# Performance work log

Hardware: AMD Instinct MI355X
Metric: run time of the kernel (lower is better)

## Reference

```python
import jax, jax.numpy as jnp
import numpy as np

B, N, C = 32, 1000, 81
MAX_INST = 100
MIN_CONF = 0.7
NMS_THRESH = 0.3
WINDOW = (0.0, 0.0, 1.0, 1.0)  # normalized y1, x1, y2, x2


def _apply_deltas(boxes, deltas):
    # boxes, deltas: [N, 4] in (y1, x1, y2, x2) / (dy, dx, log_dh, log_dw)
    h = boxes[:, 2] - boxes[:, 0]
    w = boxes[:, 3] - boxes[:, 1]
    cy = boxes[:, 0] + 0.5 * h + deltas[:, 0] * h
    cx = boxes[:, 1] + 0.5 * w + deltas[:, 1] * w
    h = h * jnp.exp(deltas[:, 2])
    w = w * jnp.exp(deltas[:, 3])
    y1 = cy - 0.5 * h
    x1 = cx - 0.5 * w
    return jnp.stack([y1, x1, y1 + h, x1 + w], axis=1)


def _clip_boxes(boxes, window):
    wy1, wx1, wy2, wx2 = window
    return jnp.stack([
        jnp.clip(boxes[:, 0], wy1, wy2),
        jnp.clip(boxes[:, 1], wx1, wx2),
        jnp.clip(boxes[:, 2], wy1, wy2),
        jnp.clip(boxes[:, 3], wx1, wx2)], axis=1)


def _pairwise_iou(b):
    y1, x1, y2, x2 = b[:, 0], b[:, 1], b[:, 2], b[:, 3]
    area = (y2 - y1) * (x2 - x1)
    iy = jnp.maximum(jnp.minimum(y2[:, None], y2[None, :]) - jnp.maximum(y1[:, None], y1[None, :]), 0.0)
    ix = jnp.maximum(jnp.minimum(x2[:, None], x2[None, :]) - jnp.maximum(x1[:, None], x1[None, :]), 0.0)
    inter = iy * ix
    union = area[:, None] + area[None, :] - inter
    return inter / jnp.maximum(union, 1e-8)


def _refine_one(rois, probs, deltas, std_dev):
    n = rois.shape[0]
    class_ids = jnp.argmax(probs, axis=1)                 # [N]
    scores = jnp.max(probs, axis=1)                       # [N]
    # per-roi deltas for the predicted class, scaled by bbox_std_dev
    d = jnp.take_along_axis(deltas, class_ids[:, None, None], axis=1)[:, 0, :] * std_dev
    boxes = _clip_boxes(_apply_deltas(rois, d), WINDOW)   # [N, 4]
    valid = (class_ids > 0) & (scores >= MIN_CONF)        # drop background + low conf

    # sort by score descending (invalid at the end)
    order = jnp.argsort(-jnp.where(valid, scores, -jnp.inf))
    b = boxes[order]
    s = scores[order]
    c = class_ids[order]
    v = valid[order]

    # greedy per-class NMS on score-sorted boxes
    iou = _pairwise_iou(b)                                # [N, N]
    sup = (iou > NMS_THRESH) & (c[:, None] == c[None, :])
    idx = jnp.arange(n)

    def step(keep, i):
        row = sup[i] & (idx > i) & keep[i]
        return keep & ~row, None

    keep, _ = jax.lax.scan(step, v, jnp.arange(n))
    keep = jax.lax.stop_gradient(keep)

    # kept boxes are already score-ordered -> compact first MAX_INST into slots
    slot = jnp.where(keep, jnp.cumsum(keep) - 1, MAX_INST)
    slot = jnp.minimum(slot, MAX_INST)                    # overflow bucket
    rows = jnp.concatenate([b, c[:, None].astype(b.dtype), s[:, None]], axis=1)  # [N, 6]
    out = jnp.zeros((MAX_INST + 1, 6), b.dtype).at[slot].set(rows)[:MAX_INST]
    return out                                            # [MAX_INST, 6]


def setup_inputs() -> dict:
    key = jax.random.key(0)
    k1, k2, k3, k4, k5 = jax.random.split(key, 5)
    cy = jax.random.uniform(k1, (B, N))
    cx = jax.random.uniform(k2, (B, N))
    h = jax.random.uniform(k3, (B, N), minval=0.02, maxval=0.4)
    w = jax.random.uniform(k4, (B, N), minval=0.02, maxval=0.4)
    rois = jnp.stack([
        jnp.clip(cy - 0.5 * h, 0.0, 1.0),
        jnp.clip(cx - 0.5 * w, 0.0, 1.0),
        jnp.clip(cy + 0.5 * h, 0.0, 1.0),
        jnp.clip(cx + 0.5 * w, 0.0, 1.0)], axis=2).astype(jnp.float32)
    logits = jax.random.normal(k5, (B, N, C), dtype=jnp.float32) * 2.0
    mrcnn_class = jax.nn.softmax(logits, axis=-1)
    mrcnn_bbox = jax.random.normal(jax.random.fold_in(key, 7), (B, N, C, 4), dtype=jnp.float32)
    bbox_std_dev = jnp.array([0.1, 0.1, 0.2, 0.2], dtype=jnp.float32)
    return {"rois": rois, "mrcnn_class": mrcnn_class, "mrcnn_bbox": mrcnn_bbox, "bbox_std_dev": bbox_std_dev}


def reference(rois, mrcnn_class, mrcnn_bbox, bbox_std_dev):
    out = jax.vmap(lambda r, p, d: _refine_one(r, p, d, bbox_std_dev))(rois, mrcnn_class, mrcnn_bbox)
    return out.reshape(B, MAX_INST, 6)
```

## Files before the change

### kernel.cpp

```cpp
#include <hip/hip_runtime.h>
#include <math.h>

#define BB 32
#define NN 1000
#define CC 81
#define MAX_INST 100
#define MIN_CONF 0.7f
#define NMS_THRESH 0.3f
#define MCAP 1024
#define RCHUNK 192
#define WMAX 16


__global__ __launch_bounds__(256) void roi_kernel(
    const float* __restrict__ rois,
    const float* __restrict__ probs,
    const float* __restrict__ deltas,
    const float* __restrict__ std_dev,
    float* __restrict__ glist,
    float* __restrict__ out)
{
  if (blockIdx.x == 0) {
    float4* o4 = (float4*)out;
    for (int i = threadIdx.x; i < BB * MAX_INST * 6 / 4; i += 256)
      o4[i] = make_float4(0.f, 0.f, 0.f, 0.f);
  }

  int wg = blockIdx.x * 4 + (threadIdx.x >> 6);
  if (wg >= BB * NN) return;
  int lane = threadIdx.x & 63;

  const float* p = probs + (size_t)wg * CC;
  float v = p[lane];
  int   c = lane;
  if (lane + 64 < CC) {
    float v2 = p[lane + 64];
    if (v2 > v) { v = v2; c = lane + 64; }
  }
  for (int off = 32; off; off >>= 1) {
    float vo = __shfl_down(v, off);
    int   co = __shfl_down(c, off);
    if (vo > v || (vo == v && co < c)) { v = vo; c = co; }
  }

  if (lane == 0) {
    float4* o = (float4*)(glist + (size_t)wg * 8);
    bool valid = (c > 0) && (v >= MIN_CONF);
    if (valid) {
      float4 dd = *(const float4*)(deltas + ((size_t)wg * CC + c) * 4);
      float4 r4 = *(const float4*)(rois + (size_t)wg * 4);
      float dy = dd.x * std_dev[0], dx = dd.y * std_dev[1];
      float dh = dd.z * std_dev[2], dw = dd.w * std_dev[3];
      float h = r4.z - r4.x, w = r4.w - r4.y;
      float cy = r4.x + 0.5f * h + dy * h;
      float cx = r4.y + 0.5f * w + dx * w;
      h *= expf(dh); w *= expf(dw);
      float y1 = cy - 0.5f * h, x1 = cx - 0.5f * w;
      float y2 = y1 + h,        x2 = x1 + w;
      y1 = fminf(fmaxf(y1, 0.f), 1.f); x1 = fminf(fmaxf(x1, 0.f), 1.f);
      y2 = fminf(fmaxf(y2, 0.f), 1.f); x2 = fminf(fmaxf(x2, 0.f), 1.f);
      o[0] = make_float4(y1, x1, y2, x2);
    }
    int b = wg / NN, n = wg - b * NN;
    o[1] = make_float4(valid ? v : -1.0f, (float)c, (float)n, 0.f);
  }
}

__global__ __launch_bounds__(256) void nms_kernel(
    const float* __restrict__ glist,
    float* __restrict__ out)
{
  const int b = blockIdx.x, t = threadIdx.x;

  __shared__ int   lcnt;
  __shared__ float cscore[MCAP];
  __shared__ int   cidx[MCAP];
  __shared__ float sy1[MCAP], sx1[MCAP], sy2[MCAP], sx2[MCAP];
  __shared__ int   scls[MCAP];
  __shared__ float sscr[MCAP];
  __shared__ unsigned long long rows[RCHUNK][WMAX];
  __shared__ unsigned long long keepw[WMAX];

  const float* base = glist + (size_t)b * NN * 8;

  if (t == 0) lcnt = 0;
  __syncthreads();

  for (int e = t; e < NN; e += 256) {
    const float4 s = ((const float4*)(base + (size_t)e * 8))[1];
    if (s.x >= 0.f) {
      int pos = atomicAdd(&lcnt, 1);
      cscore[pos] = s.x;
      cidx[pos]   = e;
    }
  }
  __syncthreads();

  const int M = lcnt;
  const int W = (M + 63) >> 6;

  for (int e = t; e < M; e += 256) {
    float sc = cscore[e]; int oi = cidx[e];
    int r = 0;
    for (int j = 0; j < M; ++j) {
      float sj = cscore[j]; int ij = cidx[j];
      if (sj > sc || (sj == sc && ij < oi)) ++r;
    }
    const float4 a = ((const float4*)(base + (size_t)oi * 8))[0];
    const float4 s = ((const float4*)(base + (size_t)oi * 8))[1];
    sy1[r] = a.x; sx1[r] = a.y; sy2[r] = a.z; sx2[r] = a.w;
    scls[r] = (int)s.y; sscr[r] = sc;
  }
  if (t < WMAX) {
    unsigned long long kw = 0ULL;
    int nb = M - t * 64;
    if (nb > 0) kw = (nb >= 64) ? ~0ULL : ((1ULL << nb) - 1ULL);
    keepw[t] = kw;
  }
  __syncthreads();

  const int wv = t >> 6, lane = t & 63;
  for (int c0 = 0; c0 < M; c0 += RCHUNK) {
    int R = min(RCHUNK, M - c0);
    for (int task = wv; task < R * W; task += 4) {
      int i = c0 + task / W;
      int w = task % W;
      int j = w * 64 + lane;
      bool cond = false;
      float iy1 = sy1[i], ix1 = sx1[i], iy2 = sy2[i], ix2 = sx2[i];
      int ic = scls[i];
      if (j < M && j > i && scls[j] == ic) {
        float jy1 = sy1[j], jx1 = sx1[j], jy2 = sy2[j], jx2 = sx2[j];
        float ai = (iy2 - iy1) * (ix2 - ix1);
        float aj = (jy2 - jy1) * (jx2 - jx1);
        float iy = fmaxf(fminf(iy2, jy2) - fmaxf(iy1, jy1), 0.f);
        float ix = fmaxf(fminf(ix2, jx2) - fmaxf(ix1, jx1), 0.f);
        float inter = iy * ix;
        float uni = fmaxf(ai + aj - inter, 1e-8f);
        cond = (inter / uni) > NMS_THRESH;
      }
      unsigned long long word = __ballot(cond);
      if (lane == 0) rows[task / W][w] = word;
    }
    __syncthreads();
    if (t < 64) {
      unsigned long long kw = (t < W) ? keepw[t] : 0ULL;
      for (int i = c0; i < c0 + R; ++i) {
        unsigned long long kwi = __shfl((long long)kw, i >> 6);
        if ((kwi >> (i & 63)) & 1ULL) {
          if (t < W) kw &= ~rows[i - c0][t];
        }
      }
      if (t < W) keepw[t] = kw;
    }
    __syncthreads();
  }

  for (int r = t; r < M; r += 256) {
    unsigned long long kwme = keepw[r >> 6];
    if ((kwme >> (r & 63)) & 1ULL) {
      int slot = 0;
      for (int w = 0; w < (r >> 6); ++w) slot += __popcll(keepw[w]);
      slot += __popcll(kwme & ((1ULL << (r & 63)) - 1ULL));
      if (slot < MAX_INST) {
        float* o = out + ((size_t)b * MAX_INST + slot) * 6;
        o[0] = sy1[r]; o[1] = sx1[r]; o[2] = sy2[r]; o[3] = sx2[r];
        o[4] = (float)scls[r]; o[5] = sscr[r];
      }
    }
  }
}

extern "C" void kernel_launch(void* const* d_in, const int* in_sizes, int n_in,
                              void* d_out, int out_size, void* d_ws, size_t ws_size,
                              hipStream_t stream) {
  const float* rois    = (const float*)d_in[0];
  const float* probs   = (const float*)d_in[1];
  const float* deltas  = (const float*)d_in[2];
  const float* std_dev = (const float*)d_in[3];
  float* out = (float*)d_out;

  float* glist = (float*)d_ws;

  roi_kernel<<<(BB * NN + 3) / 4, 256, 0, stream>>>(rois, probs, deltas, std_dev,
                                                    glist, out);
  nms_kernel<<<BB, 256, 0, stream>>>(glist, out);
}
```

Measured before the change: 103.8 us.

## Split ROI output into SoA buffers, use half-wave argmax, add single-wave NMS path

The ROI kernel now reduces each row over 32 lanes instead of 64, so 8 rows are processed per block. It writes scores, classes and boxes into separate struct-of-arrays buffers rather than an interleaved 8-float record. The NMS kernel loads scores as float4 vectors, zeroes its own slice of the output, and uses a serial single-wave greedy path with no block barriers when at most 64 candidates survive. Together these aim to cut memory traffic, launch work and synchronisation. The fast path only runs when the candidate count is small, which depends on the input distribution.

```diff
diff --git a/kernel.cpp b/kernel.cpp
--- a/kernel.cpp
+++ b/kernel.cpp
@@ -17,35 +17,32 @@
     const float* __restrict__ probs,
     const float* __restrict__ deltas,
     const float* __restrict__ std_dev,
-    float* __restrict__ glist,
-    float* __restrict__ out)
+    float* __restrict__ sval,
+    int* __restrict__ gcls,
+    float4* __restrict__ gbox)
 {
-  if (blockIdx.x == 0) {
-    float4* o4 = (float4*)out;
-    for (int i = threadIdx.x; i < BB * MAX_INST * 6 / 4; i += 256)
-      o4[i] = make_float4(0.f, 0.f, 0.f, 0.f);
-  }
-
-  int wg = blockIdx.x * 4 + (threadIdx.x >> 6);
+  int wg = blockIdx.x * 8 + (threadIdx.x >> 5);
   if (wg >= BB * NN) return;
-  int lane = threadIdx.x & 63;
+  int hl = threadIdx.x & 31;
 
   const float* p = probs + (size_t)wg * CC;
-  float v = p[lane];
-  int   c = lane;
-  if (lane + 64 < CC) {
-    float v2 = p[lane + 64];
-    if (v2 > v) { v = v2; c = lane + 64; }
-  }
-  for (int off = 32; off; off >>= 1) {
+  float v = p[hl];
+  int   c = hl;
+  float v2 = p[hl + 32];
+  if (v2 > v) { v = v2; c = hl + 32; }
+  if (hl < CC - 64) {
+    float v3 = p[hl + 64];
+    if (v3 > v) { v = v3; c = hl + 64; }
+  }
+  for (int off = 16; off; off >>= 1) {
     float vo = __shfl_down(v, off);
     int   co = __shfl_down(c, off);
     if (vo > v || (vo == v && co < c)) { v = vo; c = co; }
   }
 
-  if (lane == 0) {
-    float4* o = (float4*)(glist + (size_t)wg * 8);
+  if (hl == 0) {
     bool valid = (c > 0) && (v >= MIN_CONF);
+    sval[wg] = valid ? v : -1.0f;
     if (valid) {
       float4 dd = *(const float4*)(deltas + ((size_t)wg * CC + c) * 4);
       float4 r4 = *(const float4*)(rois + (size_t)wg * 4);
@@ -59,58 +56,102 @@
       float y2 = y1 + h,        x2 = x1 + w;
       y1 = fminf(fmaxf(y1, 0.f), 1.f); x1 = fminf(fmaxf(x1, 0.f), 1.f);
       y2 = fminf(fmaxf(y2, 0.f), 1.f); x2 = fminf(fmaxf(x2, 0.f), 1.f);
-      o[0] = make_float4(y1, x1, y2, x2);
-    }
-    int b = wg / NN, n = wg - b * NN;
-    o[1] = make_float4(valid ? v : -1.0f, (float)c, (float)n, 0.f);
+      gcls[wg] = c;
+      gbox[wg] = make_float4(y1, x1, y2, x2);
+    }
   }
 }
 
 __global__ __launch_bounds__(256) void nms_kernel(
-    const float* __restrict__ glist,
+    const float* __restrict__ sval,
+    const int* __restrict__ gcls,
+    const float4* __restrict__ gbox,
     float* __restrict__ out)
 {
   const int b = blockIdx.x, t = threadIdx.x;
 
   __shared__ int   lcnt;
-  __shared__ float cscore[MCAP];
-  __shared__ int   cidx[MCAP];
+  __shared__ float lscore[MCAP];
+  __shared__ int   lidx[MCAP];
   __shared__ float sy1[MCAP], sx1[MCAP], sy2[MCAP], sx2[MCAP];
-  __shared__ int   scls[MCAP];
+  __shared__ int   scl[MCAP];
   __shared__ float sscr[MCAP];
   __shared__ unsigned long long rows[RCHUNK][WMAX];
   __shared__ unsigned long long keepw[WMAX];
 
-  const float* base = glist + (size_t)b * NN * 8;
+  float4* ob4 = (float4*)(out + (size_t)b * MAX_INST * 6);
+  for (int i = t; i < MAX_INST * 6 / 4; i += 256)
+    ob4[i] = make_float4(0.f, 0.f, 0.f, 0.f);
 
   if (t == 0) lcnt = 0;
   __syncthreads();
 
-  for (int e = t; e < NN; e += 256) {
-    const float4 s = ((const float4*)(base + (size_t)e * 8))[1];
-    if (s.x >= 0.f) {
-      int pos = atomicAdd(&lcnt, 1);
-      cscore[pos] = s.x;
-      cidx[pos]   = e;
-    }
+  const float4* sv4 = (const float4*)(sval + (size_t)b * NN);
+  if (t < NN / 4) {
+    float4 s4 = sv4[t];
+    if (s4.x >= 0.f) { int q = atomicAdd(&lcnt, 1); lscore[q] = s4.x; lidx[q] = 4 * t + 0; }
+    if (s4.y >= 0.f) { int q = atomicAdd(&lcnt, 1); lscore[q] = s4.y; lidx[q] = 4 * t + 1; }
+    if (s4.z >= 0.f) { int q = atomicAdd(&lcnt, 1); lscore[q] = s4.z; lidx[q] = 4 * t + 2; }
+    if (s4.w >= 0.f) { int q = atomicAdd(&lcnt, 1); lscore[q] = s4.w; lidx[q] = 4 * t + 3; }
   }
   __syncthreads();
 
   const int M = lcnt;
-  const int W = (M + 63) >> 6;
+  const size_t boff = (size_t)b * NN;
 
   for (int e = t; e < M; e += 256) {
-    float sc = cscore[e]; int oi = cidx[e];
+    float sc = lscore[e]; int oi = lidx[e];
     int r = 0;
     for (int j = 0; j < M; ++j) {
-      float sj = cscore[j]; int ij = cidx[j];
+      float sj = lscore[j]; int ij = lidx[j];
       if (sj > sc || (sj == sc && ij < oi)) ++r;
     }
-    const float4 a = ((const float4*)(base + (size_t)oi * 8))[0];
-    const float4 s = ((const float4*)(base + (size_t)oi * 8))[1];
+    float4 a = gbox[boff + oi];
     sy1[r] = a.x; sx1[r] = a.y; sy2[r] = a.z; sx2[r] = a.w;
-    scls[r] = (int)s.y; sscr[r] = sc;
-  }
+    scl[r] = gcls[boff + oi]; sscr[r] = sc;
+  }
+  __syncthreads();
+
+  if (M <= 64) {
+    if (t < 64) {
+      const int j = t;
+      float jy1 = 0.f, jx1 = 0.f, jy2 = 0.f, jx2 = 0.f, aj = 0.f, jscr = 0.f;
+      int jc = -1;
+      if (j < M) {
+        jy1 = sy1[j]; jx1 = sx1[j]; jy2 = sy2[j]; jx2 = sx2[j];
+        jc = scl[j]; jscr = sscr[j];
+        aj = (jy2 - jy1) * (jx2 - jx1);
+      }
+      unsigned long long keep = (M >= 64) ? ~0ULL : ((1ULL << M) - 1ULL);
+      for (int i = 0; i < M; ++i) {
+        if ((keep >> i) & 1ULL) {
+          float iy1 = sy1[i], ix1 = sx1[i], iy2 = sy2[i], ix2 = sx2[i];
+          int   ic  = scl[i];
+          float ai  = (iy2 - iy1) * (ix2 - ix1);
+          bool cond = false;
+          if (j > i && j < M && jc == ic) {
+            float iy = fmaxf(fminf(iy2, jy2) - fmaxf(iy1, jy1), 0.f);
+            float ix = fmaxf(fminf(ix2, jx2) - fmaxf(ix1, jx1), 0.f);
+            float inter = iy * ix;
+            float uni = fmaxf(ai + aj - inter, 1e-8f);
+            cond = (inter / uni) > NMS_THRESH;
+          }
+          keep &= ~__ballot(cond);
+        }
+      }
+      if (j < M && ((keep >> j) & 1ULL)) {
+        int slot = __popcll(keep & ((1ULL << j) - 1ULL));
+        if (slot < MAX_INST) {
+          float* o = out + ((size_t)b * MAX_INST + slot) * 6;
+          o[0] = jy1; o[1] = jx1; o[2] = jy2; o[3] = jx2;
+          o[4] = (float)jc; o[5] = jscr;
+        }
+      }
+    }
+    return;
+  }
+
+  const int W = (M + 63) >> 6;
   if (t < WMAX) {
     unsigned long long kw = 0ULL;
     int nb = M - t * 64;
@@ -128,8 +169,8 @@
       int j = w * 64 + lane;
       bool cond = false;
       float iy1 = sy1[i], ix1 = sx1[i], iy2 = sy2[i], ix2 = sx2[i];
-      int ic = scls[i];
-      if (j < M && j > i && scls[j] == ic) {
+      int ic = scl[i];
+      if (j < M && j > i && scl[j] == ic) {
         float jy1 = sy1[j], jx1 = sx1[j], jy2 = sy2[j], jx2 = sx2[j];
         float ai = (iy2 - iy1) * (ix2 - ix1);
         float aj = (jy2 - jy1) * (jx2 - jx1);
@@ -165,7 +206,7 @@
       if (slot < MAX_INST) {
         float* o = out + ((size_t)b * MAX_INST + slot) * 6;
         o[0] = sy1[r]; o[1] = sx1[r]; o[2] = sy2[r]; o[3] = sx2[r];
-        o[4] = (float)scls[r]; o[5] = sscr[r];
+        o[4] = (float)scl[r]; o[5] = sscr[r];
       }
     }
   }
@@ -180,9 +221,11 @@
   const float* std_dev = (const float*)d_in[3];
   float* out = (float*)d_out;
 
-  float* glist = (float*)d_ws;
-
-  roi_kernel<<<(BB * NN + 3) / 4, 256, 0, stream>>>(rois, probs, deltas, std_dev,
-                                                    glist, out);
-  nms_kernel<<<BB, 256, 0, stream>>>(glist, out);
+  float*  sval = (float*)d_ws;
+  int*    gcls = (int*)((char*)d_ws + 0x20000);
+  float4* gbox = (float4*)((char*)d_ws + 0x40000);
+
+  roi_kernel<<<(BB * NN + 7) / 8, 256, 0, stream>>>(rois, probs, deltas, std_dev,
+                                                    sval, gcls, gbox);
+  nms_kernel<<<BB, 256, 0, stream>>>(sval, gcls, gbox, out);
 }
```

After: 98.91 us, median of 2. 4.7% less time.
